# Kernel tuning notes

Measured on AMD Instinct MI355X. Metric: run time of the kernel, lower is better.

The kernel has to match this reference:

```python
import jax, jax.numpy as jnp
import numpy as np

jax.config.update("jax_enable_x64", True)  # original uses .double() for the partition function

B, L, NS = 32768, 16, 1024  # batch, n_labels, n_legal_states


def setup_inputs() -> dict:
    key = jax.random.key(0)
    kf, ky, ks = jax.random.split(key, 3)
    f = jax.random.normal(kf, (B, L), dtype=jnp.float32)
    y = jax.random.uniform(ky, (B, L), dtype=jnp.float32)  # soft labels in [0,1]
    S = jax.random.randint(ks, (NS, L), 0, 2).astype(jnp.int32)  # binary legal-state matrix
    return {"f": f, "y": y, "S": S}


def _focal_fidelity(p, g, gamma=2.0, alpha=0.75, eps=1e-8):
    p = p.reshape(-1)
    g = g.reshape(-1)
    fidelity = jnp.sqrt(p * g + eps) + jnp.sqrt((1.0 - p) * (1.0 - g) + eps)
    p_t = p * g + (1.0 - p) * (1.0 - g)
    alpha_t = alpha * g + (1.0 - alpha) * (1.0 - g)
    loss = (1.0 - fidelity) * alpha_t * (1.0 - p_t) ** gamma
    return jnp.mean(loss)


def reference(f, y, S):
    Sd = S.astype(jnp.float64)                      # [NS, L]
    potential = Sd @ f.T.astype(jnp.float64)        # [NS, B]
    max_sf = jnp.max(potential, axis=0)             # [B]
    J = jnp.exp(potential - max_sf)                 # [NS, B]
    z = jnp.sum(J, axis=0)                          # [B]
    # fused batched segment-reduce over states: indicator.T @ J replaces the per-column loop
    num = (S > 0).astype(jnp.float64).T @ J         # [L, B]
    pMargin = (num / z).T.astype(jnp.float32)       # [B, L]
    all_loss = _focal_fidelity(pMargin, y)
    return all_loss, pMargin
```

## Files before the change

### kernel.cpp

```cpp
#include <hip/hip_runtime.h>
#include <math.h>

#define LBL 16
#define B_TOTAL 32768
#define WAVES 16
#define BLOCK_THREADS 1024
#define COLS_PER_BLOCK 128
#define GRID_BLOCKS (B_TOTAL / COLS_PER_BLOCK)

#define SCM_WOFF 8192
#define SCM_STRIDE 516
#define LDS_WORDS (SCM_WOFF + LBL * SCM_STRIDE)

typedef __attribute__((ext_vector_type(8))) short bf16x8;
typedef __attribute__((ext_vector_type(4))) float f32x4;

#define LOG2E 1.4426950408889634f

#if __has_builtin(__builtin_amdgcn_exp2f)
#define EXP2F __builtin_amdgcn_exp2f
#else
#define EXP2F exp2f
#endif

static __device__ __forceinline__ unsigned short bf16_rne(float x) {
    union { float f; unsigned u; } v; v.f = x;
    unsigned r = v.u + 0x7FFFu + ((v.u >> 16) & 1u);
    return (unsigned short)(r >> 16);
}
static __device__ __forceinline__ float bf16_to_f(unsigned short h) {
    union { unsigned u; float f; } v; v.u = ((unsigned)h) << 16;
    return v.f;
}
static __device__ __forceinline__ unsigned cvt_pk_bf16(float lo, float hi) {
    unsigned r;
    asm("v_cvt_pk_bf16_f32 %0, %1, %2" : "=v"(r) : "v"(lo), "v"(hi));
    return r;
}

#define PKB(p, q) ((((p) > 0) ? 0x3F80u : 0u) | (((q) > 0) ? 0x3F800000u : 0u))

__global__ __launch_bounds__(BLOCK_THREADS, 4) void plm_mfma8(
    const float* __restrict__ f, const float* __restrict__ y,
    const int* __restrict__ S, float* __restrict__ out,
    float* __restrict__ block_loss)
{
    __shared__ __align__(16) unsigned SH[LDS_WORDS];
    __shared__ float wls[WAVES];
    unsigned short* U16 = (unsigned short*)SH;
    float* part = (float*)SH;

    const int tid = threadIdx.x;

    const int w = tid >> 6, lane = tid & 63;
    const int c = lane & 15;
    const int g = lane >> 4;
    const int cg = w & 7;
    const int half = w >> 3;
    const int b = blockIdx.x * COLS_PER_BLOCK + cg * LBL + c;
    const int h = g & 1;
    const int hilo = g >> 1;

    const float4* fr = (const float4*)(f + (size_t)b * LBL + h * 8);
    float4 x0 = fr[0], x1 = fr[1];

    if (tid < 512) {
        const int s0 = tid * 2;
        int b0[16], b1[16];
        {
            const int4* sp = (const int4*)(S + (size_t)s0 * LBL);
            int4 a = sp[0], bq = sp[1], cq = sp[2], dq = sp[3];
            b0[0]=a.x;  b0[1]=a.y;  b0[2]=a.z;  b0[3]=a.w;
            b0[4]=bq.x; b0[5]=bq.y; b0[6]=bq.z; b0[7]=bq.w;
            b0[8]=cq.x; b0[9]=cq.y; b0[10]=cq.z;b0[11]=cq.w;
            b0[12]=dq.x;b0[13]=dq.y;b0[14]=dq.z;b0[15]=dq.w;
        }
        {
            const int4* sp = (const int4*)(S + (size_t)(s0 + 1) * LBL);
            int4 a = sp[0], bq = sp[1], cq = sp[2], dq = sp[3];
            b1[0]=a.x;  b1[1]=a.y;  b1[2]=a.z;  b1[3]=a.w;
            b1[4]=bq.x; b1[5]=bq.y; b1[6]=bq.z; b1[7]=bq.w;
            b1[8]=cq.x; b1[9]=cq.y; b1[10]=cq.z;b1[11]=cq.w;
            b1[12]=dq.x;b1[13]=dq.y;b1[14]=dq.z;b1[15]=dq.w;
        }
        const int half_s = s0 >> 9, tt = (s0 >> 5) & 15, o = s0 & 31;
        const int q = (o >> 2) & 1;
        const int x = ((o >> 4) & 1) * 8 + ((o >> 3) & 1) * 4 + (o & 3);
        const int slot = half_s * 512 + tt * 32 + q * 16 + x;
        unsigned short* Urow = U16 + slot * 16;
        uint4 ua = { PKB(b0[0],b0[1]),  PKB(b0[2],b0[3]),  PKB(b0[4],b0[5]),  PKB(b0[6],b0[7]) };
        uint4 ub = { PKB(b0[8],b0[9]),  PKB(b0[10],b0[11]),PKB(b0[12],b0[13]),PKB(b0[14],b0[15]) };
        uint4 uc = { PKB(b1[0],b1[1]),  PKB(b1[2],b1[3]),  PKB(b1[4],b1[5]),  PKB(b1[6],b1[7]) };
        uint4 ud = { PKB(b1[8],b1[9]),  PKB(b1[10],b1[11]),PKB(b1[12],b1[13]),PKB(b1[14],b1[15]) };
        *(uint4*)&Urow[0]  = ua;
        *(uint4*)&Urow[8]  = ub;
        *(uint4*)&Urow[16] = uc;
        *(uint4*)&Urow[24] = ud;
#pragma unroll
        for (int l = 0; l < 16; ++l) {
            unsigned v = (((b0[l] > 0) ? 0x3F80u : 0u)) | (((b1[l] > 0) ? 0x3F800000u : 0u));
            SH[SCM_WOFF + l * SCM_STRIDE + ((unsigned)tid ^ ((unsigned)(l & 3) << 2))] = v;
        }
    }
    __syncthreads();

    float xs[8] = { x0.x, x0.y, x0.z, x0.w, x1.x, x1.y, x1.z, x1.w };
#pragma unroll
    for (int j = 0; j < 8; ++j) xs[j] *= LOG2E;

    float up = 0.f;
#pragma unroll
    for (int j = 0; j < 8; ++j) up += fmaxf(xs[j], 0.f);
    const float U2 = up + __shfl_xor(up, 16);
    const float nUb = -U2;
    const f32x4 cin = { nUb, nUb, nUb, nUb };

    union { unsigned short s[8]; bf16x8 v; } b1u;
#pragma unroll
    for (int j = 0; j < 8; ++j) {
        unsigned short hb = bf16_rne(xs[j]);
        unsigned short lb = bf16_rne(xs[j] - bf16_to_f(hb));
        b1u.s[j] = (unsigned short)(hilo ? lb : hb);
    }
    const bf16x8 b1f = b1u.v;

    const unsigned gc = (unsigned)(g ^ (c & 3));
    const char* baseA  = (const char*)SH + half * 16384 + 32 * c + 16 * h;
    const char* baseS2 = (const char*)SH + SCM_WOFF * 4 + 2064 * c + 1024 * half + 16 * gc;

    f32x4 cacc = 0.0f;
    float zacc = 0.f;

#pragma unroll 4
    for (int t = 0; t < 16; ++t) {
        const char* pa = baseA + t * 1024;
        bf16x8 A0 = *(const bf16x8*)(pa);
        bf16x8 A1 = *(const bf16x8*)(pa + 512);
        bf16x8 a2 = *(const bf16x8*)(baseS2 + t * 64);

        f32x4 pot0 = __builtin_amdgcn_mfma_f32_16x16x32_bf16(A0, b1f, cin, 0, 0, 0);
        f32x4 pot1 = __builtin_amdgcn_mfma_f32_16x16x32_bf16(A1, b1f, cin, 0, 0, 0);

        float e0 = EXP2F(pot0[0]), e1 = EXP2F(pot0[1]);
        float e2 = EXP2F(pot0[2]), e3 = EXP2F(pot0[3]);
        float e4 = EXP2F(pot1[0]), e5 = EXP2F(pot1[1]);
        float e6 = EXP2F(pot1[2]), e7 = EXP2F(pot1[3]);
        zacc += ((e0 + e1) + (e2 + e3)) + ((e4 + e5) + (e6 + e7));

        union { unsigned u[4]; bf16x8 v; } b2;
        b2.u[0] = cvt_pk_bf16(e0, e1);
        b2.u[1] = cvt_pk_bf16(e2, e3);
        b2.u[2] = cvt_pk_bf16(e4, e5);
        b2.u[3] = cvt_pk_bf16(e6, e7);

        cacc = __builtin_amdgcn_mfma_f32_16x16x32_bf16(a2, b2.v, cacc, 0, 0, 0);
    }

    __syncthreads();
    *(f32x4*)&part[(w * 16 + c) * 20 + 4 * g] = cacc;
    part[(w * 16 + c) * 20 + 16 + g] = zacc;
    __syncthreads();

    {
        const int cg2 = tid >> 7;
        const int c2  = (tid >> 3) & 15;
        const int lp  = tid & 7;
        const int w0 = cg2, w1 = cg2 + 8;
        const int bg = blockIdx.x * COLS_PER_BLOCK + cg2 * LBL + c2;

        float z = 0.f;
#pragma unroll
        for (int gg = 0; gg < 4; ++gg)
            z += part[(w0 * 16 + c2) * 20 + 16 + gg] + part[(w1 * 16 + c2) * 20 + 16 + gg];
        const float invz = 1.0f / z;

        const float2 yv = *(const float2*)(y + (size_t)bg * LBL + 2 * lp);
        float yr[2] = { yv.x, yv.y };
        float* prow = out + 1 + (size_t)bg * LBL + 2 * lp;

        float ls = 0.f;
#pragma unroll
        for (int r2 = 0; r2 < 2; ++r2) {
            const int l = 2 * lp + r2;
            float num = part[(w0 * 16 + c2) * 20 + l] + part[(w1 * 16 + c2) * 20 + l];
            float p = num * invz;
            prow[r2] = p;
            float gv = yr[r2];
            float fid = sqrtf(fmaf(p, gv, 1e-8f)) + sqrtf(fmaf(1.f - p, 1.f - gv, 1e-8f));
            float pt = fmaf(p, gv, (1.f - p) * (1.f - gv));
            float at = fmaf(0.75f, gv, 0.25f * (1.f - gv));
            float om = 1.f - pt;
            ls += (1.f - fid) * at * om * om;
        }
#pragma unroll
        for (int off = 32; off; off >>= 1) ls += __shfl_down(ls, off);
        if (lane == 0) wls[w] = ls;
    }
    __syncthreads();
    if (tid == 0) {
        float t = 0.f;
#pragma unroll
        for (int i = 0; i < WAVES; ++i) t += wls[i];
        block_loss[blockIdx.x] = t;
    }
}

__global__ __launch_bounds__(256) void plm_reduce(
    const float* __restrict__ block_loss, int n, float* __restrict__ out)
{
    __shared__ float wsum[4];
    float s = 0.f;
    for (int i = threadIdx.x; i < n; i += 256) s += block_loss[i];
#pragma unroll
    for (int off = 32; off; off >>= 1) s += __shfl_down(s, off);
    const int wave = threadIdx.x >> 6;
    if ((threadIdx.x & 63) == 0) wsum[wave] = s;
    __syncthreads();
    if (threadIdx.x == 0) {
        float t = (wsum[0] + wsum[1]) + (wsum[2] + wsum[3]);
        out[0] = t * (1.0f / ((float)B_TOTAL * (float)LBL));
    }
}

extern "C" void kernel_launch(void* const* d_in, const int* in_sizes, int n_in,
                              void* d_out, int out_size, void* d_ws, size_t ws_size,
                              hipStream_t stream) {
    const float* f = (const float*)d_in[0];
    const float* y = (const float*)d_in[1];
    const int*   S = (const int*)d_in[2];
    float* out = (float*)d_out;
    float* bl  = (float*)d_ws;

    plm_mfma8<<<GRID_BLOCKS, BLOCK_THREADS, 0, stream>>>(f, y, S, out, bl);
    plm_reduce<<<1, 256, 0, stream>>>(bl, GRID_BLOCKS, out);
}
```

Baseline: 16.15 us.

## Switch to 32x32x16 MFMA tiles with ones-row partition sum and bitmask S staging

```diff
diff --git a/kernel.cpp b/kernel.cpp
--- a/kernel.cpp
+++ b/kernel.cpp
@@ -8,12 +8,14 @@
 #define COLS_PER_BLOCK 128
 #define GRID_BLOCKS (B_TOTAL / COLS_PER_BLOCK)
 
-#define SCM_WOFF 8192
-#define SCM_STRIDE 516
-#define LDS_WORDS (SCM_WOFF + LBL * SCM_STRIDE)
-
-typedef __attribute__((ext_vector_type(8))) short bf16x8;
-typedef __attribute__((ext_vector_type(4))) float f32x4;
+#define U_BOFF     0
+#define A2_BOFF    32768
+#define SMASK_BOFF 98304
+#define LDS_BYTES  102400
+
+typedef __attribute__((ext_vector_type(8)))  short bf16x8;
+typedef __attribute__((ext_vector_type(4)))  float f32x4;
+typedef __attribute__((ext_vector_type(16))) float f32x16;
 
 #define LOG2E 1.4426950408889634f
 
@@ -38,152 +40,166 @@
     return r;
 }
 
-#define PKB(p, q) ((((p) > 0) ? 0x3F80u : 0u) | (((q) > 0) ? 0x3F800000u : 0u))
-
-__global__ __launch_bounds__(BLOCK_THREADS, 4) void plm_mfma8(
+#define PKB2(m, l) (((((m) >> (l)) & 1u) ? 0x3F80u : 0u) | ((((m) >> ((l) + 1)) & 1u) ? 0x3F800000u : 0u))
+#define PKR(a, b, r) (((((a) >> (r)) & 1u) ? 0x3F80u : 0u) | ((((b) >> (r)) & 1u) ? 0x3F800000u : 0u))
+
+__global__ __launch_bounds__(BLOCK_THREADS, 4) void plm_mfma10(
     const float* __restrict__ f, const float* __restrict__ y,
     const int* __restrict__ S, float* __restrict__ out,
     float* __restrict__ block_loss)
 {
-    __shared__ __align__(16) unsigned SH[LDS_WORDS];
+    __shared__ __align__(16) unsigned char SHB[LDS_BYTES];
     __shared__ float wls[WAVES];
-    unsigned short* U16 = (unsigned short*)SH;
-    float* part = (float*)SH;
+    unsigned* SH = (unsigned*)SHB;
 
     const int tid = threadIdx.x;
-
     const int w = tid >> 6, lane = tid & 63;
-    const int c = lane & 15;
-    const int g = lane >> 4;
-    const int cg = w & 7;
-    const int half = w >> 3;
-    const int b = blockIdx.x * COLS_PER_BLOCK + cg * LBL + c;
-    const int h = g & 1;
-    const int hilo = g >> 1;
-
-    const float4* fr = (const float4*)(f + (size_t)b * LBL + h * 8);
-    float4 x0 = fr[0], x1 = fr[1];
-
-    if (tid < 512) {
-        const int s0 = tid * 2;
-        int b0[16], b1[16];
-        {
-            const int4* sp = (const int4*)(S + (size_t)s0 * LBL);
-            int4 a = sp[0], bq = sp[1], cq = sp[2], dq = sp[3];
-            b0[0]=a.x;  b0[1]=a.y;  b0[2]=a.z;  b0[3]=a.w;
-            b0[4]=bq.x; b0[5]=bq.y; b0[6]=bq.z; b0[7]=bq.w;
-            b0[8]=cq.x; b0[9]=cq.y; b0[10]=cq.z;b0[11]=cq.w;
-            b0[12]=dq.x;b0[13]=dq.y;b0[14]=dq.z;b0[15]=dq.w;
+    const int qt = w >> 2;
+    const int cg = w & 3;
+    const int col = lane & 31;
+    const int kh = lane >> 5;
+    const int b = blockIdx.x * COLS_PER_BLOCK + cg * 32 + col;
+
+    const int lp = tid & 7;
+    const int col128 = tid >> 3;
+    const int bg = blockIdx.x * COLS_PER_BLOCK + col128;
+    const float2 yv = *(const float2*)(y + (size_t)bg * LBL + 2 * lp);
+
+    const float4* fr = (const float4*)(f + (size_t)b * LBL + kh * 8);
+    float4 fx0 = fr[0], fx1 = fr[1];
+
+    {
+        const int s = tid;
+        const int4* sp = (const int4*)(S + (size_t)s * LBL);
+        int4 ra = sp[0], rb = sp[1], rc = sp[2], rd = sp[3];
+        unsigned m = (ra.x>0?1u:0u)       | ((ra.y>0?1u:0u)<<1)  | ((ra.z>0?1u:0u)<<2)  | ((ra.w>0?1u:0u)<<3)
+                   | ((rb.x>0?1u:0u)<<4)  | ((rb.y>0?1u:0u)<<5)  | ((rb.z>0?1u:0u)<<6)  | ((rb.w>0?1u:0u)<<7)
+                   | ((rc.x>0?1u:0u)<<8)  | ((rc.y>0?1u:0u)<<9)  | ((rc.z>0?1u:0u)<<10) | ((rc.w>0?1u:0u)<<11)
+                   | ((rd.x>0?1u:0u)<<12) | ((rd.y>0?1u:0u)<<13) | ((rd.z>0?1u:0u)<<14) | ((rd.w>0?1u:0u)<<15);
+        const int qts = s >> 8, ts = (s >> 5) & 7, o = s & 31;
+        const int x = (o & 3) | (((o >> 2) & 1) << 3) | (((o >> 3) & 1) << 2) | (o & 16);
+        unsigned* Uw = SH + ((U_BOFF + qts * 8192 + ts * 1024 + x * 32) >> 2);
+        uint4 w0 = { PKB2(m, 0), PKB2(m, 2),  PKB2(m, 4),  PKB2(m, 6)  };
+        uint4 w1 = { PKB2(m, 8), PKB2(m, 10), PKB2(m, 12), PKB2(m, 14) };
+        *(uint4*)Uw       = w0;
+        *(uint4*)(Uw + 4) = w1;
+        SH[(SMASK_BOFF >> 2) + s] = m;
+    }
+    __syncthreads();
+
+    {
+        const int frag = tid >> 4;
+        const int rp = tid & 15;
+        const unsigned* mk = SH + (SMASK_BOFF >> 2) + frag * 16;
+        uint4 q0 = *(const uint4*)(mk),     q1 = *(const uint4*)(mk + 4);
+        uint4 q2 = *(const uint4*)(mk + 8), q3 = *(const uint4*)(mk + 12);
+        unsigned mm[16] = { q0.x,q0.y,q0.z,q0.w, q1.x,q1.y,q1.z,q1.w,
+                            q2.x,q2.y,q2.z,q2.w, q3.x,q3.y,q3.z,q3.w };
+        unsigned* A2w = SH + ((A2_BOFF + frag * 1024 + rp * 64) >> 2);
+#pragma unroll
+        for (int rr = 0; rr < 2; ++rr) {
+            const int r = rp * 2 + rr;
+            uint4 lo, hi;
+            if (r < 16) {
+                lo = (uint4){ PKR(mm[0],mm[1],r),   PKR(mm[2],mm[3],r),
+                              PKR(mm[4],mm[5],r),   PKR(mm[6],mm[7],r) };
+                hi = (uint4){ PKR(mm[8],mm[9],r),   PKR(mm[10],mm[11],r),
+                              PKR(mm[12],mm[13],r), PKR(mm[14],mm[15],r) };
+            } else if (r == 16) {
+                lo = (uint4){0x3F803F80u,0x3F803F80u,0x3F803F80u,0x3F803F80u};
+                hi = lo;
+            } else {
+                lo = (uint4){0u,0u,0u,0u};
+                hi = lo;
+            }
+            *(uint4*)(A2w + rr * 8)     = lo;
+            *(uint4*)(A2w + rr * 8 + 4) = hi;
         }
-        {
-            const int4* sp = (const int4*)(S + (size_t)(s0 + 1) * LBL);
-            int4 a = sp[0], bq = sp[1], cq = sp[2], dq = sp[3];
-            b1[0]=a.x;  b1[1]=a.y;  b1[2]=a.z;  b1[3]=a.w;
-            b1[4]=bq.x; b1[5]=bq.y; b1[6]=bq.z; b1[7]=bq.w;
-            b1[8]=cq.x; b1[9]=cq.y; b1[10]=cq.z;b1[11]=cq.w;
-            b1[12]=dq.x;b1[13]=dq.y;b1[14]=dq.z;b1[15]=dq.w;
-        }
-        const int half_s = s0 >> 9, tt = (s0 >> 5) & 15, o = s0 & 31;
-        const int q = (o >> 2) & 1;
-        const int x = ((o >> 4) & 1) * 8 + ((o >> 3) & 1) * 4 + (o & 3);
-        const int slot = half_s * 512 + tt * 32 + q * 16 + x;
-        unsigned short* Urow = U16 + slot * 16;
-        uint4 ua = { PKB(b0[0],b0[1]),  PKB(b0[2],b0[3]),  PKB(b0[4],b0[5]),  PKB(b0[6],b0[7]) };
-        uint4 ub = { PKB(b0[8],b0[9]),  PKB(b0[10],b0[11]),PKB(b0[12],b0[13]),PKB(b0[14],b0[15]) };
-        uint4 uc = { PKB(b1[0],b1[1]),  PKB(b1[2],b1[3]),  PKB(b1[4],b1[5]),  PKB(b1[6],b1[7]) };
-        uint4 ud = { PKB(b1[8],b1[9]),  PKB(b1[10],b1[11]),PKB(b1[12],b1[13]),PKB(b1[14],b1[15]) };
-        *(uint4*)&Urow[0]  = ua;
-        *(uint4*)&Urow[8]  = ub;
-        *(uint4*)&Urow[16] = uc;
-        *(uint4*)&Urow[24] = ud;
-#pragma unroll
-        for (int l = 0; l < 16; ++l) {
-            unsigned v = (((b0[l] > 0) ? 0x3F80u : 0u)) | (((b1[l] > 0) ? 0x3F800000u : 0u));
-            SH[SCM_WOFF + l * SCM_STRIDE + ((unsigned)tid ^ ((unsigned)(l & 3) << 2))] = v;
-        }
-    }
-    __syncthreads();
-
-    float xs[8] = { x0.x, x0.y, x0.z, x0.w, x1.x, x1.y, x1.z, x1.w };
+    }
+    __syncthreads();
+
+    float xs[8] = { fx0.x, fx0.y, fx0.z, fx0.w, fx1.x, fx1.y, fx1.z, fx1.w };
 #pragma unroll
     for (int j = 0; j < 8; ++j) xs[j] *= LOG2E;
 
     float up = 0.f;
 #pragma unroll
     for (int j = 0; j < 8; ++j) up += fmaxf(xs[j], 0.f);
-    const float U2 = up + __shfl_xor(up, 16);
+    const float U2 = up + __shfl_xor(up, 32);
     const float nUb = -U2;
-    const f32x4 cin = { nUb, nUb, nUb, nUb };
-
-    union { unsigned short s[8]; bf16x8 v; } b1u;
+    f32x16 cin;
+#pragma unroll
+    for (int j = 0; j < 16; ++j) cin[j] = nUb;
+
+    union { unsigned short s[8]; bf16x8 v; } bhi, blo;
 #pragma unroll
     for (int j = 0; j < 8; ++j) {
         unsigned short hb = bf16_rne(xs[j]);
         unsigned short lb = bf16_rne(xs[j] - bf16_to_f(hb));
-        b1u.s[j] = (unsigned short)(hilo ? lb : hb);
-    }
-    const bf16x8 b1f = b1u.v;
-
-    const unsigned gc = (unsigned)(g ^ (c & 3));
-    const char* baseA  = (const char*)SH + half * 16384 + 32 * c + 16 * h;
-    const char* baseS2 = (const char*)SH + SCM_WOFF * 4 + 2064 * c + 1024 * half + 16 * gc;
-
-    f32x4 cacc = 0.0f;
-    float zacc = 0.f;
-
-#pragma unroll 4
-    for (int t = 0; t < 16; ++t) {
-        const char* pa = baseA + t * 1024;
-        bf16x8 A0 = *(const bf16x8*)(pa);
-        bf16x8 A1 = *(const bf16x8*)(pa + 512);
-        bf16x8 a2 = *(const bf16x8*)(baseS2 + t * 64);
-
-        f32x4 pot0 = __builtin_amdgcn_mfma_f32_16x16x32_bf16(A0, b1f, cin, 0, 0, 0);
-        f32x4 pot1 = __builtin_amdgcn_mfma_f32_16x16x32_bf16(A1, b1f, cin, 0, 0, 0);
-
-        float e0 = EXP2F(pot0[0]), e1 = EXP2F(pot0[1]);
-        float e2 = EXP2F(pot0[2]), e3 = EXP2F(pot0[3]);
-        float e4 = EXP2F(pot1[0]), e5 = EXP2F(pot1[1]);
-        float e6 = EXP2F(pot1[2]), e7 = EXP2F(pot1[3]);
-        zacc += ((e0 + e1) + (e2 + e3)) + ((e4 + e5) + (e6 + e7));
-
-        union { unsigned u[4]; bf16x8 v; } b2;
-        b2.u[0] = cvt_pk_bf16(e0, e1);
-        b2.u[1] = cvt_pk_bf16(e2, e3);
-        b2.u[2] = cvt_pk_bf16(e4, e5);
-        b2.u[3] = cvt_pk_bf16(e6, e7);
-
-        cacc = __builtin_amdgcn_mfma_f32_16x16x32_bf16(a2, b2.v, cacc, 0, 0, 0);
-    }
-
-    __syncthreads();
-    *(f32x4*)&part[(w * 16 + c) * 20 + 4 * g] = cacc;
-    part[(w * 16 + c) * 20 + 16 + g] = zacc;
-    __syncthreads();
-
-    {
-        const int cg2 = tid >> 7;
-        const int c2  = (tid >> 3) & 15;
-        const int lp  = tid & 7;
-        const int w0 = cg2, w1 = cg2 + 8;
-        const int bg = blockIdx.x * COLS_PER_BLOCK + cg2 * LBL + c2;
-
-        float z = 0.f;
-#pragma unroll
-        for (int gg = 0; gg < 4; ++gg)
-            z += part[(w0 * 16 + c2) * 20 + 16 + gg] + part[(w1 * 16 + c2) * 20 + 16 + gg];
+        bhi.s[j] = hb; blo.s[j] = lb;
+    }
+    const bf16x8 b1hi = bhi.v, b1lo = blo.v;
+
+    const char* pU  = (const char*)SHB + U_BOFF  + qt * 8192  + col * 32 + kh * 16;
+    const char* pA2 = (const char*)SHB + A2_BOFF + qt * 16384 + col * 32 + kh * 16;
+
+    f32x16 cacc = 0.0f;
+
+#pragma unroll
+    for (int t = 0; t < 8; ++t) {
+        bf16x8 A1  = *(const bf16x8*)(pU + t * 1024);
+        bf16x8 A2a = *(const bf16x8*)(pA2 + t * 2048);
+        bf16x8 A2b = *(const bf16x8*)(pA2 + t * 2048 + 1024);
+
+        f32x16 pot = __builtin_amdgcn_mfma_f32_32x32x16_bf16(A1, b1lo, cin, 0, 0, 0);
+        pot        = __builtin_amdgcn_mfma_f32_32x32x16_bf16(A1, b1hi, pot, 0, 0, 0);
+
+        float e[16];
+#pragma unroll
+        for (int r = 0; r < 16; ++r) e[r] = EXP2F(pot[r]);
+
+        union { unsigned u[4]; bf16x8 v; } b2a, b2b;
+        b2a.u[0] = cvt_pk_bf16(e[0], e[1]);   b2a.u[1] = cvt_pk_bf16(e[2], e[3]);
+        b2a.u[2] = cvt_pk_bf16(e[4], e[5]);   b2a.u[3] = cvt_pk_bf16(e[6], e[7]);
+        b2b.u[0] = cvt_pk_bf16(e[8], e[9]);   b2b.u[1] = cvt_pk_bf16(e[10], e[11]);
+        b2b.u[2] = cvt_pk_bf16(e[12], e[13]); b2b.u[3] = cvt_pk_bf16(e[14], e[15]);
+
+        cacc = __builtin_amdgcn_mfma_f32_32x32x16_bf16(A2a, b2a.v, cacc, 0, 0, 0);
+        cacc = __builtin_amdgcn_mfma_f32_32x32x16_bf16(A2b, b2b.v, cacc, 0, 0, 0);
+    }
+
+    __syncthreads();
+    {
+        float* pc = (float*)SHB + (w * 32 + col) * 20 + kh * 4;
+        f32x4 v0 = { cacc[0], cacc[1], cacc[2], cacc[3] };
+        f32x4 v1 = { cacc[4], cacc[5], cacc[6], cacc[7] };
+        *(f32x4*)pc       = v0;
+        *(f32x4*)(pc + 8) = v1;
+        if (!kh) pc[16] = cacc[8];
+    }
+    __syncthreads();
+
+    {
+        const int cg2 = col128 >> 5, c32 = col128 & 31;
+        const float* pp = (const float*)SHB;
+        const int l0 = 2 * lp, l1 = l0 + 1;
+        float z = 0.f, n0 = 0.f, n1 = 0.f;
+#pragma unroll
+        for (int q2 = 0; q2 < 4; ++q2) {
+            const int base = ((q2 * 4 + cg2) * 32 + c32) * 20;
+            z  += pp[base + 16];
+            n0 += pp[base + l0];
+            n1 += pp[base + l1];
+        }
         const float invz = 1.0f / z;
-
-        const float2 yv = *(const float2*)(y + (size_t)bg * LBL + 2 * lp);
+        float* prow = out + 1 + (size_t)bg * LBL + 2 * lp;
+
+        float nn[2] = { n0, n1 };
         float yr[2] = { yv.x, yv.y };
-        float* prow = out + 1 + (size_t)bg * LBL + 2 * lp;
-
         float ls = 0.f;
 #pragma unroll
         for (int r2 = 0; r2 < 2; ++r2) {
-            const int l = 2 * lp + r2;
-            float num = part[(w0 * 16 + c2) * 20 + l] + part[(w1 * 16 + c2) * 20 + l];
-            float p = num * invz;
+            float p = nn[r2] * invz;
             prow[r2] = p;
             float gv = yr[r2];
             float fid = sqrtf(fmaf(p, gv, 1e-8f)) + sqrtf(fmaf(1.f - p, 1.f - gv, 1e-8f));
@@ -231,6 +247,6 @@
     float* out = (float*)d_out;
     float* bl  = (float*)d_ws;
 
-    plm_mfma8<<<GRID_BLOCKS, BLOCK_THREADS, 0, stream>>>(f, y, S, out, bl);
+    plm_mfma10<<<GRID_BLOCKS, BLOCK_THREADS, 0, stream>>>(f, y, S, out, bl);
     plm_reduce<<<1, 256, 0, stream>>>(bl, GRID_BLOCKS, out);
 }
```

After: 15.48 us. -4.1%, faster.
